# Kernel tuning notes

Hardware: AMD Instinct MI355X
Metric: run time of the kernel (lower is better)

Reference implementation:

```python
import jax, jax.numpy as jnp
import numpy as np

B, S, E = 2, 2048, 2048
H, DH = 16, 128          # n_head, head_dim
ROT = 32                 # rotary_dim (partial RoPE)
MP = 8                   # mp_num in original forward
MASKED_BIAS = -1e9


def setup_inputs() -> dict:
    key = jax.random.key(0)
    k1, k2, k3 = jax.random.split(key, 3)
    hidden_states = jax.random.normal(k1, (B, S, E), dtype=jnp.float32)
    W_qkv = jax.random.normal(k2, (3 * E, E), dtype=jnp.float32) * (E ** -0.5)
    W_out = jax.random.normal(k3, (E, E), dtype=jnp.float32) * (E ** -0.5)
    return {"hidden_states": hidden_states, "W_qkv": W_qkv, "W_out": W_out}


def _rope_sincos(seq_len, rot_dim, dtype):
    inv_freq = 1.0 / (10000.0 ** (jnp.arange(0, rot_dim, 2, dtype=jnp.float32) / rot_dim))
    ang = jnp.arange(seq_len, dtype=jnp.float32)[:, None] * inv_freq[None, :]  # [S, R/2]
    return jnp.sin(ang).astype(dtype), jnp.cos(ang).astype(dtype)


def _apply_rope(x, sin, cos):
    # x: [B,S,H,R]; sin/cos: [S,R/2] -> repeat_interleave(2) -> [S,R]
    sin2 = jnp.repeat(sin, 2, axis=-1)[None, :, None, :]
    cos2 = jnp.repeat(cos, 2, axis=-1)[None, :, None, :]
    x1 = x[..., ::2]
    x2 = x[..., 1::2]
    rot = jnp.stack((-x2, x1), axis=-1).reshape(x.shape)  # rotate_every_two
    return x * cos2 + rot * sin2


def reference(hidden_states, W_qkv, W_out):
    b, s, e = hidden_states.shape
    # qkv_proj (no bias): torch Linear does x @ W^T
    qkv = jnp.einsum('bse,fe->bsf', hidden_states, W_qkv)          # [B,S,3E]
    qkv = qkv.reshape(b, s, MP, 3 * e // MP)
    q, k, v = jnp.split(qkv, 3, axis=-1)                            # each [B,S,MP,E/MP]
    # _split_heads: flatten mp dim, re-split into heads
    q = q.reshape(b, s, H, DH)
    k = k.reshape(b, s, H, DH)
    v = v.reshape(b, s, H, DH)
    # partial rotary on first ROT dims (q,k in [B,S,H,DH] layout)
    sin, cos = _rope_sincos(s, ROT, hidden_states.dtype)
    q = jnp.concatenate([_apply_rope(q[..., :ROT], sin, cos), q[..., ROT:]], axis=-1)
    k = jnp.concatenate([_apply_rope(k[..., :ROT], sin, cos), k[..., ROT:]], axis=-1)
    # attention: scores / sqrt(DH), causal masked_fill(-1e9), softmax, AV
    scale = jnp.sqrt(jnp.asarray(DH, dtype=jnp.float32)).astype(hidden_states.dtype)
    scores = jnp.einsum('bqhd,bkhd->bhqk', q, k) / scale            # [B,H,S,S]
    causal = jnp.tril(jnp.ones((s, s), dtype=bool))
    scores = jnp.where(causal[None, None], scores, jnp.asarray(MASKED_BIAS, scores.dtype))
    attn = jax.nn.softmax(scores, axis=-1)
    out = jnp.einsum('bhqk,bkhd->bqhd', attn, v)                    # [B,S,H,DH]
    out = out.reshape(b, s, e)
    return jnp.einsum('bse,fe->bsf', out, W_out)                    # out_proj
```

## Files before the change

kernel.cpp:

```cpp
#include <hip/hip_runtime.h>
#include <hip/hip_bf16.h>
#include <cstdint>
#include <cstddef>

using bf16 = __hip_bfloat16;
using short4v = __attribute__((ext_vector_type(4))) short;
using short8 = __attribute__((ext_vector_type(8))) short;
using floatx4 = __attribute__((ext_vector_type(4))) float;

#define MFMA_BF16(A, B, C) __builtin_amdgcn_mfma_f32_16x16x32_bf16((A), (B), (C), 0, 0, 0)

__device__ inline short bf16_bits(float x) {
  bf16 v = __float2bfloat16(x);
  short r;
  __builtin_memcpy(&r, &v, 2);
  return r;
}

__device__ inline void store_c(bf16* p, float v) { *p = __float2bfloat16(v); }
__device__ inline void store_c(float* p, float v) { *p = v; }

__global__ __launch_bounds__(256) void f32_to_bf16_kernel(
    const float* __restrict__ src, bf16* __restrict__ dst, int n8) {
  const int i = blockIdx.x * 256 + threadIdx.x;
  if (i >= n8) return;
  const float4 a = ((const float4*)src)[2 * i];
  const float4 b = ((const float4*)src)[2 * i + 1];
  short8 r;
  r[0] = bf16_bits(a.x); r[1] = bf16_bits(a.y); r[2] = bf16_bits(a.z); r[3] = bf16_bits(a.w);
  r[4] = bf16_bits(b.x); r[5] = bf16_bits(b.y); r[6] = bf16_bits(b.z); r[7] = bf16_bits(b.w);
  *(short8*)(dst + (size_t)i * 8) = r;
}

template <typename TC>
__global__ __launch_bounds__(256) void gemm_bt_async(
    const bf16* __restrict__ A, const bf16* __restrict__ B, TC* __restrict__ C,
    int ldc, int K) {
  __shared__ bf16 As[128 * 64];
  __shared__ bf16 Bs[128 * 64];
  const int tid = threadIdx.x;
  const int lane = tid & 63;
  const int wave = tid >> 6;
  const int lrow = lane & 15;
  const int quad = lane >> 4;
  const int wm = (wave >> 1) * 64;
  const int wn = (wave & 1) * 64;
  const int tm = blockIdx.y * 128;
  const int tn = blockIdx.x * 128;

  const int srow = tid >> 3;
  const int scl = tid & 7;

  floatx4 acc[4][4] = {};

  for (int k0 = 0; k0 < K; k0 += 64) {
    __syncthreads();
#pragma unroll
    for (int r = 0; r < 4; ++r) {
      const int row = r * 32 + srow;
      const int scg = scl ^ (row & 7);
      __builtin_amdgcn_global_load_lds(
          (const __attribute__((address_space(1))) void*)(A + (size_t)(tm + row) * K + k0 + scg * 8),
          (__attribute__((address_space(3))) void*)(As + row * 64 + scl * 8), 16, 0, 0);
    }
#pragma unroll
    for (int r = 0; r < 4; ++r) {
      const int row = r * 32 + srow;
      const int scg = scl ^ (row & 7);
      __builtin_amdgcn_global_load_lds(
          (const __attribute__((address_space(1))) void*)(B + (size_t)(tn + row) * K + k0 + scg * 8),
          (__attribute__((address_space(3))) void*)(Bs + row * 64 + scl * 8), 16, 0, 0);
    }
    __syncthreads();

#pragma unroll
    for (int kk = 0; kk < 2; ++kk) {
      short8 af[4], bfr[4];
#pragma unroll
      for (int i = 0; i < 4; ++i) {
        const int ra = wm + i * 16 + lrow;
        const int rb = wn + i * 16 + lrow;
        af[i] = *(const short8*)&As[ra * 64 + (((kk * 4 + quad) ^ (ra & 7)) * 8)];
        bfr[i] = *(const short8*)&Bs[rb * 64 + (((kk * 4 + quad) ^ (rb & 7)) * 8)];
      }
#pragma unroll
      for (int i = 0; i < 4; ++i)
#pragma unroll
        for (int j = 0; j < 4; ++j)
          acc[i][j] = MFMA_BF16(af[i], bfr[j], acc[i][j]);
    }
  }

#pragma unroll
  for (int i = 0; i < 4; ++i)
#pragma unroll
    for (int j = 0; j < 4; ++j)
#pragma unroll
      for (int r = 0; r < 4; ++r) {
        const int row = tm + wm + i * 16 + quad * 4 + r;
        const int col = tn + wn + j * 16 + lrow;
        store_c(&C[(size_t)row * ldc + col], acc[i][j][r]);
      }
}

__global__ __launch_bounds__(256) void gemm_abf16_bf32(
    const bf16* __restrict__ A, const float* __restrict__ B, float* __restrict__ C,
    int ldc, int K) {
  __shared__ bf16 As[128 * 64];
  __shared__ bf16 Bs[128 * 64];
  const int tid = threadIdx.x;
  const int lane = tid & 63;
  const int wave = tid >> 6;
  const int lrow = lane & 15;
  const int quad = lane >> 4;
  const int wm = (wave >> 1) * 64;
  const int wn = (wave & 1) * 64;
  const int tm = blockIdx.y * 128;
  const int tn = blockIdx.x * 128;

  const int srow = tid >> 3;
  const int scl = tid & 7;
  const int c16 = tid & 15;
  const int br0 = tid >> 4;

  floatx4 acc[4][4] = {};
  float4 breg[8];
#pragma unroll
  for (int r = 0; r < 8; ++r)
    breg[r] = *(const float4*)(B + (size_t)(tn + r * 16 + br0) * K + c16 * 4);

  for (int k0 = 0; k0 < K; k0 += 64) {
    __syncthreads();
#pragma unroll
    for (int r = 0; r < 4; ++r) {
      const int row = r * 32 + srow;
      const int scg = scl ^ (row & 7);
      __builtin_amdgcn_global_load_lds(
          (const __attribute__((address_space(1))) void*)(A + (size_t)(tm + row) * K + k0 + scg * 8),
          (__attribute__((address_space(3))) void*)(As + row * 64 + scl * 8), 16, 0, 0);
    }
#pragma unroll
    for (int r = 0; r < 8; ++r) {
      const int row = r * 16 + br0;
      short4v sv;
      sv[0] = bf16_bits(breg[r].x); sv[1] = bf16_bits(breg[r].y);
      sv[2] = bf16_bits(breg[r].z); sv[3] = bf16_bits(breg[r].w);
      *(short4v*)&Bs[row * 64 + (((c16 >> 1) ^ (row & 7)) * 8) + (c16 & 1) * 4] = sv;
    }
    __syncthreads();
    if (k0 + 64 < K) {
#pragma unroll
      for (int r = 0; r < 8; ++r)
        breg[r] = *(const float4*)(B + (size_t)(tn + r * 16 + br0) * K + k0 + 64 + c16 * 4);
    }

#pragma unroll
    for (int kk = 0; kk < 2; ++kk) {
      short8 af[4], bfr[4];
#pragma unroll
      for (int i = 0; i < 4; ++i) {
        const int ra = wm + i * 16 + lrow;
        const int rb = wn + i * 16 + lrow;
        af[i] = *(const short8*)&As[ra * 64 + (((kk * 4 + quad) ^ (ra & 7)) * 8)];
        bfr[i] = *(const short8*)&Bs[rb * 64 + (((kk * 4 + quad) ^ (rb & 7)) * 8)];
      }
#pragma unroll
      for (int i = 0; i < 4; ++i)
#pragma unroll
        for (int j = 0; j < 4; ++j)
          acc[i][j] = MFMA_BF16(af[i], bfr[j], acc[i][j]);
    }
  }

#pragma unroll
  for (int i = 0; i < 4; ++i)
#pragma unroll
    for (int j = 0; j < 4; ++j)
#pragma unroll
      for (int r = 0; r < 4; ++r) {
        const int row = tm + wm + i * 16 + quad * 4 + r;
        const int col = tn + wn + j * 16 + lrow;
        C[(size_t)row * ldc + col] = acc[i][j][r];
      }
}

__global__ void rope_kernel(bf16* __restrict__ qkv) {
  const int idx = blockIdx.x * 256 + threadIdx.x;
  const int i = idx & 15;
  int t = idx >> 4;
  const int qk = t & 1;
  t >>= 1;
  const int h = t & 15;
  t >>= 4;
  const int s = t & 2047;
  bf16* p = qkv + (size_t)t * 6144 + (h >> 1) * 768 + (h & 1) * 128 + qk * 256 + 2 * i;
  const float x0 = __bfloat162float(p[0]);
  const float x1 = __bfloat162float(p[1]);
  const float inv = powf(10000.f, -(float)(2 * i) / 32.f);
  const float ang = (float)s * inv;
  float sn, cs;
  sincosf(ang, &sn, &cs);
  p[0] = __float2bfloat16(x0 * cs - x1 * sn);
  p[1] = __float2bfloat16(x1 * cs + x0 * sn);
}

__global__ __launch_bounds__(256) void attn_flash_pair(
    const bf16* __restrict__ qkv, bf16* __restrict__ out) {
  __shared__ short Ks[16 * 64 * 8];
  __shared__ short Vs[8 * 128 * 8];
  __shared__ short Ps[8 * 128 * 8];
  const int tid = threadIdx.x;
  const int wave = tid >> 6;
  const int lane = tid & 63;
  const int lrow = lane & 15;
  const int quad = lane >> 4;
  const int h = blockIdx.y;
  const int b = blockIdx.z;
  const size_t SROW = 6144;
  const bf16* base = qkv + (size_t)b * 2048 * SROW;
  const int qoff = (h >> 1) * 768 + (h & 1) * 128;
  const int koff = qoff + 256;
  const int voff = qoff + 512;
  const float scale = 0.088388347648318447f;

  const int sr = tid >> 2;
  const int sq = tid & 3;

  for (int phase = 0; phase < 2; ++phase) {
    const int qb = phase ? (15 - (int)blockIdx.x) : (int)blockIdx.x;

    short8 qf[2][4];
#pragma unroll
    for (int rt = 0; rt < 2; ++rt) {
      const bf16* qp =
          base + (size_t)(qb * 128 + wave * 32 + rt * 16 + lrow) * SROW + qoff + quad * 8;
#pragma unroll
      for (int ks = 0; ks < 4; ++ks) qf[rt][ks] = *(const short8*)(qp + ks * 32);
    }

    floatx4 o[2][8] = {};
    float m_i[8], l_i[8];
#pragma unroll
    for (int i = 0; i < 8; ++i) {
      m_i[i] = -1e30f;
      l_i[i] = 0.f;
    }

    const int kb_end = qb * 2 + 2;
    for (int kb = 0; kb < kb_end; ++kb) {
      __syncthreads();
      {
        const bf16* kp = base + (size_t)(kb * 64 + sr) * SROW + koff + sq * 32;
        short8 kv[4];
#pragma unroll
        for (int j = 0; j < 4; ++j) kv[j] = *(const short8*)(kp + j * 8);
#pragma unroll
        for (int j = 0; j < 4; ++j) *(short8*)&Ks[((sq * 4 + j) * 64 + sr) * 8] = kv[j];

        const bf16* vp = base + (size_t)(kb * 64 + sr) * SROW + voff + sq * 8;
        const int so = (sr >> 3) * 128, si = sr & 7;
#pragma unroll
        for (int i = 0; i < 4; ++i) {
          short8 vv = *(const short8*)(vp + i * 32);
          const int d0 = sq * 8 + i * 32;
#pragma unroll
          for (int j = 0; j < 8; ++j) Vs[(so + d0 + j) * 8 + si] = vv[j];
        }
      }
      __syncthreads();

      floatx4 sc[2][4] = {};
#pragma unroll
      for (int ks = 0; ks < 4; ++ks) {
        short8 bfr[4];
#pragma unroll
        for (int ct = 0; ct < 4; ++ct)
          bfr[ct] = *(const short8*)&Ks[((ks * 4 + quad) * 64 + ct * 16 + lrow) * 8];
#pragma unroll
        for (int rt = 0; rt < 2; ++rt)
#pragma unroll
          for (int ct = 0; ct < 4; ++ct)
            sc[rt][ct] = MFMA_BF16(qf[rt][ks], bfr[ct], sc[rt][ct]);
      }

#pragma unroll
      for (int rt = 0; rt < 2; ++rt)
#pragma unroll
        for (int r = 0; r < 4; ++r) {
          const int idx = rt * 4 + r;
          const int row_g = qb * 128 + wave * 32 + rt * 16 + quad * 4 + r;
          float mx = -1e30f;
#pragma unroll
          for (int ct = 0; ct < 4; ++ct) {
            const int col_g = kb * 64 + ct * 16 + lrow;
            float v = sc[rt][ct][r] * scale;
            if (col_g > row_g) v = -1e9f;
            sc[rt][ct][r] = v;
            mx = fmaxf(mx, v);
          }
#pragma unroll
          for (int off = 1; off < 16; off <<= 1) mx = fmaxf(mx, __shfl_xor(mx, off, 64));
          const float mnew = fmaxf(m_i[idx], mx);
          const float alpha = __expf(m_i[idx] - mnew);
          m_i[idx] = mnew;
          float rs = 0.f;
#pragma unroll
          for (int ct = 0; ct < 4; ++ct) {
            const float p = __expf(sc[rt][ct][r] - mnew);
            sc[rt][ct][r] = p;
            rs += p;
          }
#pragma unroll
          for (int off = 1; off < 16; off <<= 1) rs += __shfl_xor(rs, off, 64);
          l_i[idx] = l_i[idx] * alpha + rs;
#pragma unroll
          for (int dt = 0; dt < 8; ++dt) o[rt][dt][r] *= alpha;
        }

#pragma unroll
      for (int rt = 0; rt < 2; ++rt)
#pragma unroll
        for (int ct = 0; ct < 4; ++ct)
#pragma unroll
          for (int r = 0; r < 4; ++r) {
            const int row_l = wave * 32 + rt * 16 + quad * 4 + r;
            const int sk = ct * 16 + lrow;
            Ps[((sk >> 3) * 128 + row_l) * 8 + (sk & 7)] = bf16_bits(sc[rt][ct][r]);
          }
      __syncthreads();

#pragma unroll
      for (int ks = 0; ks < 2; ++ks) {
        short8 af[2], bfr[8];
#pragma unroll
        for (int rt = 0; rt < 2; ++rt)
          af[rt] = *(const short8*)&Ps[((ks * 4 + quad) * 128 + wave * 32 + rt * 16 + lrow) * 8];
#pragma unroll
        for (int dt = 0; dt < 8; ++dt)
          bfr[dt] = *(const short8*)&Vs[((ks * 4 + quad) * 128 + dt * 16 + lrow) * 8];
#pragma unroll
        for (int rt = 0; rt < 2; ++rt)
#pragma unroll
          for (int dt = 0; dt < 8; ++dt)
            o[rt][dt] = MFMA_BF16(af[rt], bfr[dt], o[rt][dt]);
      }
    }

#pragma unroll
    for (int rt = 0; rt < 2; ++rt)
#pragma unroll
      for (int dt = 0; dt < 8; ++dt)
#pragma unroll
        for (int r = 0; r < 4; ++r) {
          const int row = qb * 128 + wave * 32 + rt * 16 + quad * 4 + r;
          const int d = dt * 16 + lrow;
          const float val = o[rt][dt][r] / l_i[rt * 4 + r];
          out[((size_t)(b * 2048 + row)) * 2048 + h * 128 + d] = __float2bfloat16(val);
        }
  }
}

extern "C" void kernel_launch(void* const* d_in, const int* in_sizes, int n_in,
                              void* d_out, int out_size, void* d_ws, size_t ws_size,
                              hipStream_t stream) {
  const float* hidden = (const float*)d_in[0];
  const float* Wqkv = (const float*)d_in[1];
  const float* Wout = (const float*)d_in[2];
  float* outp = (float*)d_out;

  bf16* qkv = (bf16*)d_ws;
  bf16* flex = qkv + (size_t)4096 * 6144;
  bf16* hbf = (bf16*)d_out;

  f32_to_bf16_kernel<<<4096, 256, 0, stream>>>(hidden, hbf, 1048576);

  f32_to_bf16_kernel<<<3072, 256, 0, stream>>>(Wqkv, flex, 786432);
  gemm_bt_async<bf16><<<dim3(24, 32), 256, 0, stream>>>(hbf, flex, qkv, 6144, 2048);
  f32_to_bf16_kernel<<<3072, 256, 0, stream>>>(Wqkv + (size_t)3072 * 2048, flex, 786432);
  gemm_bt_async<bf16><<<dim3(24, 32), 256, 0, stream>>>(hbf, flex, qkv + 3072, 6144, 2048);

  rope_kernel<<<8192, 256, 0, stream>>>(qkv);

  bf16* attnout = flex;
  attn_flash_pair<<<dim3(8, 16, 2), 256, 0, stream>>>(qkv, attnout);

  gemm_abf16_bf32<<<dim3(16, 32), 256, 0, stream>>>(attnout, Wout, outp, 2048, 2048);
}
```

Measured before the change: 453.8 us.

## Halve attention query tile, prefetch K/V into registers, drop P barrier

The flash attention kernel now gives each block 64 query rows instead of 128, so each wave owns one 16-row tile. The grid doubles to 512 blocks, still pairing tiles qb and 31-qb for causal load balance. The next K/V tile is loaded into registers while the current one is computed, and the barrier before the PV matmul is removed because each wave only reads its own rows of P. The causal mask is applied only on the diagonal tile, MFMA sections are wrapped in s_setprio, and normalization uses a reciprocal. The goal is more parallelism and hidden global-load latency. In exchange, each block reloads K/V twice as often, adding memory traffic, and register pressure rises from the prefetch buffers.

```diff
diff --git a/kernel.cpp b/kernel.cpp
--- a/kernel.cpp
+++ b/kernel.cpp
@@ -208,7 +208,7 @@
     const bf16* __restrict__ qkv, bf16* __restrict__ out) {
   __shared__ short Ks[16 * 64 * 8];
   __shared__ short Vs[8 * 128 * 8];
-  __shared__ short Ps[8 * 128 * 8];
+  __shared__ short Ps[8 * 64 * 8];
   const int tid = threadIdx.x;
   const int wave = tid >> 6;
   const int lane = tid & 63;
@@ -226,50 +226,64 @@
   const int sr = tid >> 2;
   const int sq = tid & 3;
 
+  const bf16* kbase = base + (size_t)sr * SROW + koff + sq * 32;
+  const bf16* vbase = base + (size_t)sr * SROW + voff + sq * 8;
+
+  short8 kv[4], vv[4];
+#pragma unroll
+  for (int j = 0; j < 4; ++j) kv[j] = *(const short8*)(kbase + j * 8);
+#pragma unroll
+  for (int i = 0; i < 4; ++i) vv[i] = *(const short8*)(vbase + i * 32);
+
   for (int phase = 0; phase < 2; ++phase) {
-    const int qb = phase ? (15 - (int)blockIdx.x) : (int)blockIdx.x;
-
-    short8 qf[2][4];
-#pragma unroll
-    for (int rt = 0; rt < 2; ++rt) {
-      const bf16* qp =
-          base + (size_t)(qb * 128 + wave * 32 + rt * 16 + lrow) * SROW + qoff + quad * 8;
-#pragma unroll
-      for (int ks = 0; ks < 4; ++ks) qf[rt][ks] = *(const short8*)(qp + ks * 32);
-    }
-
-    floatx4 o[2][8] = {};
-    float m_i[8], l_i[8];
-#pragma unroll
-    for (int i = 0; i < 8; ++i) {
+    const int qb = phase ? (31 - (int)blockIdx.x) : (int)blockIdx.x;
+
+    short8 qf[4];
+    {
+      const bf16* qp = base + (size_t)(qb * 64 + wave * 16 + lrow) * SROW + qoff + quad * 8;
+#pragma unroll
+      for (int ks = 0; ks < 4; ++ks) qf[ks] = *(const short8*)(qp + ks * 32);
+    }
+
+    floatx4 o[8] = {};
+    float m_i[4], l_i[4];
+#pragma unroll
+    for (int i = 0; i < 4; ++i) {
       m_i[i] = -1e30f;
       l_i[i] = 0.f;
     }
 
-    const int kb_end = qb * 2 + 2;
+    const int kb_end = qb + 1;
     for (int kb = 0; kb < kb_end; ++kb) {
       __syncthreads();
+
+#pragma unroll
+      for (int j = 0; j < 4; ++j) *(short8*)&Ks[((sq * 4 + j) * 64 + sr) * 8] = kv[j];
       {
-        const bf16* kp = base + (size_t)(kb * 64 + sr) * SROW + koff + sq * 32;
-        short8 kv[4];
-#pragma unroll
-        for (int j = 0; j < 4; ++j) kv[j] = *(const short8*)(kp + j * 8);
-#pragma unroll
-        for (int j = 0; j < 4; ++j) *(short8*)&Ks[((sq * 4 + j) * 64 + sr) * 8] = kv[j];
-
-        const bf16* vp = base + (size_t)(kb * 64 + sr) * SROW + voff + sq * 8;
         const int so = (sr >> 3) * 128, si = sr & 7;
 #pragma unroll
         for (int i = 0; i < 4; ++i) {
-          short8 vv = *(const short8*)(vp + i * 32);
           const int d0 = sq * 8 + i * 32;
 #pragma unroll
-          for (int j = 0; j < 8; ++j) Vs[(so + d0 + j) * 8 + si] = vv[j];
+          for (int j = 0; j < 8; ++j) Vs[(so + d0 + j) * 8 + si] = vv[i][j];
         }
       }
       __syncthreads();
 
-      floatx4 sc[2][4] = {};
+      {
+        const bool pf = (kb + 1 < kb_end) || (phase == 0);
+        const int nkb = (kb + 1 < kb_end) ? kb + 1 : 0;
+        if (pf) {
+          const size_t off = (size_t)nkb * 64 * SROW;
+#pragma unroll
+          for (int j = 0; j < 4; ++j) kv[j] = *(const short8*)(kbase + off + j * 8);
+#pragma unroll
+          for (int i = 0; i < 4; ++i) vv[i] = *(const short8*)(vbase + off + i * 32);
+        }
+      }
+
+      floatx4 sc[4] = {};
+      __builtin_amdgcn_s_setprio(1);
 #pragma unroll
       for (int ks = 0; ks < 4; ++ks) {
         short8 bfr[4];
@@ -277,86 +291,80 @@
         for (int ct = 0; ct < 4; ++ct)
           bfr[ct] = *(const short8*)&Ks[((ks * 4 + quad) * 64 + ct * 16 + lrow) * 8];
 #pragma unroll
-        for (int rt = 0; rt < 2; ++rt)
-#pragma unroll
-          for (int ct = 0; ct < 4; ++ct)
-            sc[rt][ct] = MFMA_BF16(qf[rt][ks], bfr[ct], sc[rt][ct]);
-      }
-
-#pragma unroll
-      for (int rt = 0; rt < 2; ++rt)
+        for (int ct = 0; ct < 4; ++ct)
+          sc[ct] = MFMA_BF16(qf[ks], bfr[ct], sc[ct]);
+      }
+      __builtin_amdgcn_s_setprio(0);
+
+      const bool diag = (kb == qb);
+#pragma unroll
+      for (int r = 0; r < 4; ++r) {
+        const int row_g = qb * 64 + wave * 16 + quad * 4 + r;
+        float mx = -1e30f;
+#pragma unroll
+        for (int ct = 0; ct < 4; ++ct) {
+          float v = sc[ct][r] * scale;
+          if (diag) {
+            const int col_g = kb * 64 + ct * 16 + lrow;
+            if (col_g > row_g) v = -1e9f;
+          }
+          sc[ct][r] = v;
+          mx = fmaxf(mx, v);
+        }
+#pragma unroll
+        for (int off = 1; off < 16; off <<= 1) mx = fmaxf(mx, __shfl_xor(mx, off, 64));
+        const float mnew = fmaxf(m_i[r], mx);
+        const float alpha = __expf(m_i[r] - mnew);
+        m_i[r] = mnew;
+        float rs = 0.f;
+#pragma unroll
+        for (int ct = 0; ct < 4; ++ct) {
+          const float p = __expf(sc[ct][r] - mnew);
+          sc[ct][r] = p;
+          rs += p;
+        }
+#pragma unroll
+        for (int off = 1; off < 16; off <<= 1) rs += __shfl_xor(rs, off, 64);
+        l_i[r] = l_i[r] * alpha + rs;
+#pragma unroll
+        for (int dt = 0; dt < 8; ++dt) o[dt][r] *= alpha;
+      }
+
+#pragma unroll
+      for (int ct = 0; ct < 4; ++ct)
 #pragma unroll
         for (int r = 0; r < 4; ++r) {
-          const int idx = rt * 4 + r;
-          const int row_g = qb * 128 + wave * 32 + rt * 16 + quad * 4 + r;
-          float mx = -1e30f;
-#pragma unroll
-          for (int ct = 0; ct < 4; ++ct) {
-            const int col_g = kb * 64 + ct * 16 + lrow;
-            float v = sc[rt][ct][r] * scale;
-            if (col_g > row_g) v = -1e9f;
-            sc[rt][ct][r] = v;
-            mx = fmaxf(mx, v);
-          }
-#pragma unroll
-          for (int off = 1; off < 16; off <<= 1) mx = fmaxf(mx, __shfl_xor(mx, off, 64));
-          const float mnew = fmaxf(m_i[idx], mx);
-          const float alpha = __expf(m_i[idx] - mnew);
-          m_i[idx] = mnew;
-          float rs = 0.f;
-#pragma unroll
-          for (int ct = 0; ct < 4; ++ct) {
-            const float p = __expf(sc[rt][ct][r] - mnew);
-            sc[rt][ct][r] = p;
-            rs += p;
-          }
-#pragma unroll
-          for (int off = 1; off < 16; off <<= 1) rs += __shfl_xor(rs, off, 64);
-          l_i[idx] = l_i[idx] * alpha + rs;
-#pragma unroll
-          for (int dt = 0; dt < 8; ++dt) o[rt][dt][r] *= alpha;
-        }
-
-#pragma unroll
-      for (int rt = 0; rt < 2; ++rt)
-#pragma unroll
-        for (int ct = 0; ct < 4; ++ct)
-#pragma unroll
-          for (int r = 0; r < 4; ++r) {
-            const int row_l = wave * 32 + rt * 16 + quad * 4 + r;
-            const int sk = ct * 16 + lrow;
-            Ps[((sk >> 3) * 128 + row_l) * 8 + (sk & 7)] = bf16_bits(sc[rt][ct][r]);
-          }
-      __syncthreads();
-
+          const int row_l = wave * 16 + quad * 4 + r;
+          const int sk = ct * 16 + lrow;
+          Ps[((sk >> 3) * 64 + row_l) * 8 + (sk & 7)] = bf16_bits(sc[ct][r]);
+        }
+
+      __builtin_amdgcn_s_setprio(1);
 #pragma unroll
       for (int ks = 0; ks < 2; ++ks) {
-        short8 af[2], bfr[8];
-#pragma unroll
-        for (int rt = 0; rt < 2; ++rt)
-          af[rt] = *(const short8*)&Ps[((ks * 4 + quad) * 128 + wave * 32 + rt * 16 + lrow) * 8];
+        short8 af = *(const short8*)&Ps[((ks * 4 + quad) * 64 + wave * 16 + lrow) * 8];
+        short8 bfr[8];
 #pragma unroll
         for (int dt = 0; dt < 8; ++dt)
           bfr[dt] = *(const short8*)&Vs[((ks * 4 + quad) * 128 + dt * 16 + lrow) * 8];
 #pragma unroll
-        for (int rt = 0; rt < 2; ++rt)
-#pragma unroll
-          for (int dt = 0; dt < 8; ++dt)
-            o[rt][dt] = MFMA_BF16(af[rt], bfr[dt], o[rt][dt]);
-      }
-    }
-
-#pragma unroll
-    for (int rt = 0; rt < 2; ++rt)
-#pragma unroll
-      for (int dt = 0; dt < 8; ++dt)
-#pragma unroll
-        for (int r = 0; r < 4; ++r) {
-          const int row = qb * 128 + wave * 32 + rt * 16 + quad * 4 + r;
-          const int d = dt * 16 + lrow;
-          const float val = o[rt][dt][r] / l_i[rt * 4 + r];
-          out[((size_t)(b * 2048 + row)) * 2048 + h * 128 + d] = __float2bfloat16(val);
-        }
+        for (int dt = 0; dt < 8; ++dt)
+          o[dt] = MFMA_BF16(af, bfr[dt], o[dt]);
+      }
+      __builtin_amdgcn_s_setprio(0);
+    }
+
+#pragma unroll
+    for (int r = 0; r < 4; ++r) {
+      const float inv_l = 1.f / l_i[r];
+      const int row = qb * 64 + wave * 16 + quad * 4 + r;
+#pragma unroll
+      for (int dt = 0; dt < 8; ++dt) {
+        const int d = dt * 16 + lrow;
+        out[((size_t)(b * 2048 + row)) * 2048 + h * 128 + d] =
+            __float2bfloat16(o[dt][r] * inv_l);
+      }
+    }
   }
 }
 
@@ -382,7 +390,7 @@
   rope_kernel<<<8192, 256, 0, stream>>>(qkv);
 
   bf16* attnout = flex;
-  attn_flash_pair<<<dim3(8, 16, 2), 256, 0, stream>>>(qkv, attnout);
+  attn_flash_pair<<<dim3(16, 16, 2), 256, 0, stream>>>(qkv, attnout);
 
   gemm_abf16_bf32<<<dim3(16, 32), 256, 0, stream>>>(attnout, Wout, outp, 2048, 2048);
 }
```

Result: faster. 441.2 us (-2.8%).

## Prefetch K/V tiles into registers, swizzle V/P LDS layouts, trim attention sync

Applied to the files above, without the earlier changes.

The flash-attention kernel now loads the next K/V tile from global memory into registers while MFMAs run on the current tile, instead of loading right before each LDS store. The V and P shared-memory layouts become row-major with XOR swizzles to cut bank conflicts. The barrier between writing and reading P is dropped, which is safe because each wave only touches its own rows. Further tweaks skip the causal mask outside diagonal tiles, raise wave priority around MFMA blocks, and use a reciprocal for the final normalization. The prefetch costs extra registers, which may lower occupancy.

```diff
diff --git a/kernel.cpp b/kernel.cpp
--- a/kernel.cpp
+++ b/kernel.cpp
@@ -207,8 +207,8 @@
 __global__ __launch_bounds__(256) void attn_flash_pair(
     const bf16* __restrict__ qkv, bf16* __restrict__ out) {
   __shared__ short Ks[16 * 64 * 8];
-  __shared__ short Vs[8 * 128 * 8];
-  __shared__ short Ps[8 * 128 * 8];
+  __shared__ short Vs[128 * 64];
+  __shared__ short Ps[128 * 64];
   const int tid = threadIdx.x;
   const int wave = tid >> 6;
   const int lane = tid & 63;
@@ -226,6 +226,15 @@
   const int sr = tid >> 2;
   const int sq = tid & 3;
 
+  const bf16* kbase = base + (size_t)sr * SROW + koff + sq * 32;
+  const bf16* vbase = base + (size_t)sr * SROW + voff + sq * 8;
+
+  short8 kv[4], vv[4];
+#pragma unroll
+  for (int j = 0; j < 4; ++j) kv[j] = *(const short8*)(kbase + j * 8);
+#pragma unroll
+  for (int i = 0; i < 4; ++i) vv[i] = *(const short8*)(vbase + i * 32);
+
   for (int phase = 0; phase < 2; ++phase) {
     const int qb = phase ? (15 - (int)blockIdx.x) : (int)blockIdx.x;
 
@@ -246,30 +255,42 @@
       l_i[i] = 0.f;
     }
 
-    const int kb_end = qb * 2 + 2;
+    const int kb_end = 2 * qb + 2;
     for (int kb = 0; kb < kb_end; ++kb) {
       __syncthreads();
+
+#pragma unroll
+      for (int j = 0; j < 4; ++j) *(short8*)&Ks[((sq * 4 + j) * 64 + sr) * 8] = kv[j];
       {
-        const bf16* kp = base + (size_t)(kb * 64 + sr) * SROW + koff + sq * 32;
-        short8 kv[4];
-#pragma unroll
-        for (int j = 0; j < 4; ++j) kv[j] = *(const short8*)(kp + j * 8);
-#pragma unroll
-        for (int j = 0; j < 4; ++j) *(short8*)&Ks[((sq * 4 + j) * 64 + sr) * 8] = kv[j];
-
-        const bf16* vp = base + (size_t)(kb * 64 + sr) * SROW + voff + sq * 8;
-        const int so = (sr >> 3) * 128, si = sr & 7;
+        const int kc = sr >> 3;
+        const int si = sr & 7;
 #pragma unroll
         for (int i = 0; i < 4; ++i) {
-          short8 vv = *(const short8*)(vp + i * 32);
-          const int d0 = sq * 8 + i * 32;
-#pragma unroll
-          for (int j = 0; j < 8; ++j) Vs[(so + d0 + j) * 8 + si] = vv[j];
+          const int dbase = sq * 8 + i * 32;
+          const int cc = kc ^ ((dbase >> 3) & 7);
+#pragma unroll
+          for (int j = 0; j < 8; ++j) {
+            Vs[(dbase + j) * 64 + ((cc ^ j) * 8) + si] = vv[i][j];
+          }
         }
       }
       __syncthreads();
 
+      {
+        const bool last = (kb + 1 == kb_end);
+        const bool pf = !last || (phase == 0);
+        const int nkb = !last ? kb + 1 : 0;
+        if (pf) {
+          const size_t off = (size_t)nkb * 64 * SROW;
+#pragma unroll
+          for (int j = 0; j < 4; ++j) kv[j] = *(const short8*)(kbase + off + j * 8);
+#pragma unroll
+          for (int i = 0; i < 4; ++i) vv[i] = *(const short8*)(vbase + off + i * 32);
+        }
+      }
+
       floatx4 sc[2][4] = {};
+      __builtin_amdgcn_s_setprio(1);
 #pragma unroll
       for (int ks = 0; ks < 4; ++ks) {
         short8 bfr[4];
@@ -282,19 +303,24 @@
           for (int ct = 0; ct < 4; ++ct)
             sc[rt][ct] = MFMA_BF16(qf[rt][ks], bfr[ct], sc[rt][ct]);
       }
-
+      __builtin_amdgcn_s_setprio(0);
+
+      const int wr0 = qb * 128 + wave * 32;
+      const bool diag = (kb * 64 + 63 > wr0);
 #pragma unroll
       for (int rt = 0; rt < 2; ++rt)
 #pragma unroll
         for (int r = 0; r < 4; ++r) {
           const int idx = rt * 4 + r;
-          const int row_g = qb * 128 + wave * 32 + rt * 16 + quad * 4 + r;
+          const int row_g = wr0 + rt * 16 + quad * 4 + r;
           float mx = -1e30f;
 #pragma unroll
           for (int ct = 0; ct < 4; ++ct) {
-            const int col_g = kb * 64 + ct * 16 + lrow;
             float v = sc[rt][ct][r] * scale;
-            if (col_g > row_g) v = -1e9f;
+            if (diag) {
+              const int col_g = kb * 64 + ct * 16 + lrow;
+              if (col_g > row_g) v = -1e9f;
+            }
             sc[rt][ct][r] = v;
             mx = fmaxf(mx, v);
           }
@@ -324,39 +350,49 @@
 #pragma unroll
           for (int r = 0; r < 4; ++r) {
             const int row_l = wave * 32 + rt * 16 + quad * 4 + r;
-            const int sk = ct * 16 + lrow;
-            Ps[((sk >> 3) * 128 + row_l) * 8 + (sk & 7)] = bf16_bits(sc[rt][ct][r]);
+            const int skgrp = ct * 2 + (lrow >> 3);
+            const int cc = skgrp ^ (row_l & 7);
+            Ps[row_l * 64 + cc * 8 + (lrow & 7)] = bf16_bits(sc[rt][ct][r]);
           }
-      __syncthreads();
-
+
+      __builtin_amdgcn_s_setprio(1);
 #pragma unroll
       for (int ks = 0; ks < 2; ++ks) {
         short8 af[2], bfr[8];
 #pragma unroll
-        for (int rt = 0; rt < 2; ++rt)
-          af[rt] = *(const short8*)&Ps[((ks * 4 + quad) * 128 + wave * 32 + rt * 16 + lrow) * 8];
-#pragma unroll
-        for (int dt = 0; dt < 8; ++dt)
-          bfr[dt] = *(const short8*)&Vs[((ks * 4 + quad) * 128 + dt * 16 + lrow) * 8];
+        for (int rt = 0; rt < 2; ++rt) {
+          const int row = wave * 32 + rt * 16 + lrow;
+          const int cc = (ks * 4 + quad) ^ (row & 7);
+          af[rt] = *(const short8*)&Ps[row * 64 + cc * 8];
+        }
+#pragma unroll
+        for (int dt = 0; dt < 8; ++dt) {
+          const int d = dt * 16 + lrow;
+          const int cc = ((ks * 4 + quad) ^ (d & 7) ^ ((d >> 3) & 7)) & 7;
+          bfr[dt] = *(const short8*)&Vs[d * 64 + cc * 8];
+        }
 #pragma unroll
         for (int rt = 0; rt < 2; ++rt)
 #pragma unroll
           for (int dt = 0; dt < 8; ++dt)
             o[rt][dt] = MFMA_BF16(af[rt], bfr[dt], o[rt][dt]);
       }
+      __builtin_amdgcn_s_setprio(0);
     }
 
 #pragma unroll
     for (int rt = 0; rt < 2; ++rt)
 #pragma unroll
-      for (int dt = 0; dt < 8; ++dt)
-#pragma unroll
-        for (int r = 0; r < 4; ++r) {
-          const int row = qb * 128 + wave * 32 + rt * 16 + quad * 4 + r;
+      for (int r = 0; r < 4; ++r) {
+        const float inv_l = 1.f / l_i[rt * 4 + r];
+        const int row = qb * 128 + wave * 32 + rt * 16 + quad * 4 + r;
+#pragma unroll
+        for (int dt = 0; dt < 8; ++dt) {
           const int d = dt * 16 + lrow;
-          const float val = o[rt][dt][r] / l_i[rt * 4 + r];
-          out[((size_t)(b * 2048 + row)) * 2048 + h * 128 + d] = __float2bfloat16(val);
-        }
+          out[((size_t)(b * 2048 + row)) * 2048 + h * 128 + d] =
+              __float2bfloat16(o[rt][dt][r] * inv_l);
+        }
+      }
   }
 }
 
```

Result: no change. 458.7 us (+1.1%).
